# Optimization experiments

Hardware: AMD Instinct MI355X
Metric: run time of the kernel (lower is better)

The kernel has to match this reference:

```python
import jax, jax.numpy as jnp
import numpy as np

LOSS_W = 0.6
UNC_W = 0.4
EPS = 1e-8


def setup_inputs() -> dict:
    key = jax.random.key(0)
    ks = jax.random.split(key, 6)
    B, D, C, BANK = 1024, 256, 80, 65536
    return {
        "features": jax.random.normal(ks[0], (B, D), jnp.float32),
        "predictions": jax.random.normal(ks[1], (B, C), jnp.float32),
        "targets": jax.random.uniform(ks[2], (B, C), dtype=jnp.float32),
        "query": jax.random.normal(ks[3], (B, D), jnp.float32),
        "memory": jax.random.normal(ks[4], (BANK, D), jnp.float32),
        "importance_scores": jax.random.uniform(ks[5], (BANK,), dtype=jnp.float32),
        "index": BANK,  # bank pre-filled (steady state)
        "k": 8,
    }


def _difficulty(predictions, targets):
    # per-sample BCE-with-logits, mean over classes
    bce = -(targets * jax.nn.log_sigmoid(predictions)
            + (1.0 - targets) * jax.nn.log_sigmoid(-predictions))
    sl = bce.mean(axis=1)                                   # [B]
    mx = sl.max()
    sl = jnp.where(mx > 0, sl / (mx + EPS), sl)
    probs = jax.nn.sigmoid(predictions)
    confidence = jnp.abs(probs - 0.5).mean(axis=1)
    uncertainty = jnp.clip(1.0 - 2.0 * confidence, 0.0, 1.0)
    return LOSS_W * sl + UNC_W * uncertainty                # [B]


def _update(memory, importance_scores, index, features, difficulty):
    # 'hard' mode: store samples above the 0.7 difficulty quantile,
    # sequential priority (min-replacement) insertion via scan.
    bank_size = memory.shape[0]
    thr = jnp.quantile(difficulty, 0.7)
    store = difficulty > thr                                # [B] bool

    def step(carry, inp):
        mem, scores, idx = carry
        feat, score, st = inp
        fill = idx < bank_size
        min_idx = jnp.argmin(scores)
        min_score = scores[min_idx]
        widx = jnp.where(fill, idx, min_idx)
        do_write = st & (fill | (score > min_score))
        mem = mem.at[widx].set(jnp.where(do_write, feat, mem[widx]))
        scores = scores.at[widx].set(jnp.where(do_write, score, scores[widx]))
        idx = idx + jnp.where(st & fill, 1, 0).astype(idx.dtype)
        return (mem, scores, idx), None

    init = (memory, importance_scores, jnp.asarray(index, jnp.int32))
    (mem, scores, idx), _ = jax.lax.scan(step, init, (features, difficulty, store))
    return mem, scores, idx


def _l2norm(x):
    # torch F.normalize: x / max(||x||, eps)
    n = jnp.linalg.norm(x, axis=1, keepdims=True)
    return x / jnp.maximum(n, 1e-12)


def reference(features, predictions, targets, query, memory, importance_scores, index, k):
    difficulty = _difficulty(predictions, targets)
    mem, scores, idx = _update(memory, importance_scores, index, features, difficulty)
    # retrieve: bank is full (index starts at bank_size) -> valid_size == bank_size
    sim = _l2norm(query) @ _l2norm(mem).T                   # [B, BANK]
    w, ind = jax.lax.top_k(sim, k)                          # [B, k]
    weights = jax.nn.softmax(w, axis=1)                     # [B, k]
    gathered = mem[ind]                                     # [B, k, D]
    return jnp.einsum('bk,bkd->bd', weights, gathered)      # [B, D]
```

## Files before the change

### kernel.cpp

```cpp
#include <hip/hip_runtime.h>
#include <hip/hip_bf16.h>
#include <stdint.h>

#define BANK 65536
#define BQ 1024
#define DIM 256
#define NCLS 80
#define KTOP 8
#define CAND_CAP 1024
#define SCORE_CUT 0.007f
#define NSPLIT 128
#define SPLIT_ROWS 512
#define NT 8
#define TAU 0.2f
#define SCAP 96

typedef __attribute__((ext_vector_type(8))) short short8;
typedef __attribute__((ext_vector_type(4))) float f32x4;

__device__ __forceinline__ unsigned int mono_f32(float f) {
    unsigned int b = __float_as_uint(f);
    return (b & 0x80000000u) ? ~b : (b | 0x80000000u);
}
__device__ __forceinline__ float unmono_f32(unsigned int u) {
    unsigned int b = (u & 0x80000000u) ? (u & 0x7FFFFFFFu) : ~u;
    return __uint_as_float(b);
}
__device__ __forceinline__ unsigned short f2bf(float f) {
    unsigned int u = __float_as_uint(f);
    unsigned int r = ((u >> 16) & 1u) + 0x7FFFu;
    return (unsigned short)((u + r) >> 16);
}
__device__ __forceinline__ void stage16(const char* gsrc, char* ldst) {
    __builtin_amdgcn_global_load_lds(
        (const __attribute__((address_space(1))) unsigned int*)gsrc,
        (__attribute__((address_space(3))) unsigned int*)ldst, 16, 0, 0);
}

#define INS8(L, key) do { \
    _Pragma("unroll") \
    for (int pp = 7; pp >= 1; --pp) { \
        unsigned long long prev = L[pp - 1]; \
        L[pp] = (L[pp] >= (key)) ? L[pp] : ((prev >= (key)) ? (key) : prev); \
    } \
    L[0] = (L[0] >= (key)) ? L[0] : (key); \
} while (0)

__global__ void prep_all(const float* __restrict__ memory, const float* __restrict__ features,
                         const float* __restrict__ query,
                         const float* __restrict__ pred, const float* __restrict__ targ,
                         const float* __restrict__ scores,
                         unsigned short* __restrict__ Mn, unsigned short* __restrict__ Qn,
                         float* __restrict__ invm, float* __restrict__ invq,
                         float* __restrict__ sl_raw, float* __restrict__ unc,
                         int* __restrict__ ovw, unsigned long long* __restrict__ cand,
                         int* __restrict__ meta) {
    int bx = blockIdx.x;
    if (bx < 16640) {
        int wid = threadIdx.x >> 6, lane = threadIdx.x & 63;
        int row = bx * 4 + wid;
        bool isq = (row >= BANK);
        const float* src = isq ? (query + (size_t)(row - BANK) * DIM)
                               : (memory + (size_t)row * DIM);
        float4 v = *(const float4*)(src + lane * 4);
        float ss = v.x * v.x + v.y * v.y + v.z * v.z + v.w * v.w;
        for (int off = 32; off; off >>= 1) ss += __shfl_xor(ss, off);
        float inv = 1.f / fmaxf(sqrtf(ss), 1e-12f);
        ushort4 o;
        o.x = f2bf(v.x * inv); o.y = f2bf(v.y * inv);
        o.z = f2bf(v.z * inv); o.w = f2bf(v.w * inv);
        if (!isq) {
            *(ushort4*)(Mn + (size_t)row * DIM + lane * 4) = o;
            if (lane == 0) invm[row] = inv;
        } else {
            *(ushort4*)(Qn + (size_t)(row - BANK) * DIM + lane * 4) = o;
            if (lane == 0) invq[row - BANK] = inv;
        }
    } else if (bx < 16896) {
        int wid = threadIdx.x >> 6, lane = threadIdx.x & 63;
        int b = (bx - 16640) * 4 + wid;
        float bce = 0.f, conf = 0.f;
        for (int c = lane; c < NCLS; c += 64) {
            float x = pred[b * NCLS + c];
            float t = targ[b * NCLS + c];
            float l1 = log1pf(expf(-fabsf(x)));
            float sp_pos = fmaxf(x, 0.f) + l1;
            float sp_neg = fmaxf(-x, 0.f) + l1;
            bce += t * sp_neg + (1.f - t) * sp_pos;
            float p = 1.f / (1.f + expf(-x));
            conf += fabsf(p - 0.5f);
        }
        for (int off = 32; off; off >>= 1) {
            bce += __shfl_xor(bce, off);
            conf += __shfl_xor(conf, off);
        }
        if (lane == 0) {
            sl_raw[b] = bce / (float)NCLS;
            float u = 1.f - 2.f * (conf / (float)NCLS);
            unc[b] = fminf(fmaxf(u, 0.f), 1.f);
        }
    } else {
        int i = (bx - 16896) * 256 + threadIdx.x;
        ovw[i] = -1;
        float s = scores[i];
        if (s < SCORE_CUT) {
            int pos = atomicAdd(&meta[1], 1);
            if (pos < CAND_CAP)
                cand[pos] = ((unsigned long long)__float_as_uint(s) << 32) | (unsigned long long)(unsigned)i;
        }
    }
}

__global__ void select_scatter(const float* __restrict__ sl_raw, const float* __restrict__ unc,
                               const unsigned long long* __restrict__ cand,
                               int* __restrict__ meta, int* __restrict__ ovw,
                               int* __restrict__ wlist) {
    __shared__ float red[BQ];
    __shared__ int hist[1024];
    __shared__ int pfx[1024];
    __shared__ int p[BQ];
    __shared__ int sidx[BQ];
    __shared__ int fill[1024];
    __shared__ unsigned long long kc[CAND_CAP];
    __shared__ unsigned long long buck[CAND_CAP];
    __shared__ float binvals[128];
    __shared__ int bincnt;
    __shared__ int b716s, b717s;
    __shared__ float q716s, q717s;
    int tid = threadIdx.x;

    float sl = sl_raw[tid];
    float u = unc[tid];
    red[tid] = sl;
    hist[tid] = 0;
    __syncthreads();
    for (int off = 512; off; off >>= 1) {
        if (tid < off) red[tid] = fmaxf(red[tid], red[tid + off]);
        __syncthreads();
    }
    float mx = red[0];
    float sln = (mx > 0.f) ? sl / (mx + 1e-8f) : sl;
    float diff = 0.6f * sln + 0.4f * u;
    int mybin = (int)(diff * 1024.f);
    mybin = (mybin < 0) ? 0 : ((mybin > 1023) ? 1023 : mybin);
    atomicAdd(&hist[mybin], 1);
    __syncthreads();
    pfx[tid] = hist[tid];
    __syncthreads();
    for (int off = 1; off < 1024; off <<= 1) {
        int t = (tid >= off) ? pfx[tid - off] : 0;
        __syncthreads();
        pfx[tid] += t;
        __syncthreads();
    }
    int pe = pfx[tid] - hist[tid];
    if (pe <= 716 && 716 < pfx[tid]) b716s = tid;
    if (pe <= 717 && 717 < pfx[tid]) b717s = tid;
    __syncthreads();
#pragma unroll
    for (int pass = 0; pass < 2; ++pass) {
        int target = 716 + pass;
        if (tid == 0) bincnt = 0;
        __syncthreads();
        int tb = (pass == 0) ? b716s : b717s;
        if (mybin == tb) {
            int pos = atomicAdd(&bincnt, 1);
            if (pos < 128) binvals[pos] = diff;
        }
        __syncthreads();
        if (tid == 0) {
            int bc = bincnt; if (bc > 128) bc = 128;
            for (int i = 1; i < bc; ++i) {
                float v = binvals[i]; int j = i - 1;
                while (j >= 0 && binvals[j] > v) { binvals[j + 1] = binvals[j]; --j; }
                binvals[j + 1] = v;
            }
            int base = pfx[tb] - hist[tb];
            float val = binvals[target - base];
            if (pass == 0) q716s = val; else q717s = val;
        }
        __syncthreads();
    }
    float qpos = 0.7f * (float)(BQ - 1);
    float g = qpos - floorf(qpos);
    float thr = q716s + g * (q717s - q716s);
    int flag = (diff > thr) ? 1 : 0;
    p[tid] = flag;
    __syncthreads();
    for (int off = 1; off < BQ; off <<= 1) {
        int t = (tid >= off) ? p[tid - off] : 0;
        __syncthreads();
        p[tid] += t;
        __syncthreads();
    }
    if (flag) sidx[p[tid] - 1] = tid;
    __syncthreads();
    int m = p[BQ - 1];

    int n = meta[1];
    if (n > CAND_CAP) n = CAND_CAP;
    if (m > n) m = n;
    if (tid == 0) meta[2] = m;
    kc[tid] = (tid < n) ? cand[tid] : 0xFFFFFFFFFFFFFFFFull;
    hist[tid] = 0;
    fill[tid] = 0;
    __syncthreads();
    int mybin2 = 0;
    if (tid < n) {
        float s = __uint_as_float((unsigned)(kc[tid] >> 32));
        mybin2 = (int)(s * (1024.f / SCORE_CUT));
        mybin2 = (mybin2 < 0) ? 0 : ((mybin2 > 1023) ? 1023 : mybin2);
        atomicAdd(&hist[mybin2], 1);
    }
    __syncthreads();
    pfx[tid] = hist[tid];
    __syncthreads();
    for (int off = 1; off < 1024; off <<= 1) {
        int t = (tid >= off) ? pfx[tid - off] : 0;
        __syncthreads();
        pfx[tid] += t;
        __syncthreads();
    }
    if (tid < n) {
        int pe2 = pfx[mybin2] - hist[mybin2];
        int slot = pe2 + atomicAdd(&fill[mybin2], 1);
        buck[slot] = kc[tid];
    }
    __syncthreads();
    if (tid < n) {
        int pe2 = pfx[mybin2] - hist[mybin2];
        int cnt2 = hist[mybin2];
        unsigned long long me = kc[tid];
        int rank = pe2;
        for (int i = 0; i < cnt2; ++i) rank += (buck[pe2 + i] < me) ? 1 : 0;
        if (rank < m) {
            int row = (int)(unsigned)(me & 0xFFFFFFFFu);
            ovw[row] = sidx[rank];
            wlist[rank] = row;
        }
    }
}

__global__ void patch_kernel(const float* __restrict__ features, const int* __restrict__ ovw,
                             const int* __restrict__ wlist, const int* __restrict__ meta,
                             unsigned short* __restrict__ Mn, float* __restrict__ invm) {
    int wid = threadIdx.x >> 6, lane = threadIdx.x & 63;
    int j = blockIdx.x * 4 + wid;
    if (j >= meta[2]) return;
    int row = wlist[j];
    int s = ovw[row];
    const float* src = features + (size_t)s * DIM;
    float4 v = *(const float4*)(src + lane * 4);
    float ss = v.x * v.x + v.y * v.y + v.z * v.z + v.w * v.w;
    for (int off = 32; off; off >>= 1) ss += __shfl_xor(ss, off);
    float inv = 1.f / fmaxf(sqrtf(ss), 1e-12f);
    ushort4 o;
    o.x = f2bf(v.x * inv); o.y = f2bf(v.y * inv);
    o.z = f2bf(v.z * inv); o.w = f2bf(v.w * inv);
    *(ushort4*)(Mn + (size_t)row * DIM + lane * 4) = o;
    if (lane == 0) invm[row] = inv;
}

__global__ __launch_bounds__(256, 2) void sim_coarse(
    const unsigned short* __restrict__ Qn, const unsigned short* __restrict__ Mn,
    int* __restrict__ surv, int* __restrict__ cnt) {
    __shared__ char smem[2 * 32768];

    int bx = blockIdx.x;
    int qt = bx >> 7;
    int split = bx & 127;
    int tid = threadIdx.x;
    int w = tid >> 6;
    int lane = tid & 63;
    int le = lane & 15;
    int lg = lane >> 4;
    int qbase = qt * 256 + w * 64;
    int r0 = split * SPLIT_ROWS;

    short8 qf[4][8];
#pragma unroll
    for (int qg = 0; qg < 4; ++qg)
#pragma unroll
        for (int ks = 0; ks < 8; ++ks)
            qf[qg][ks] = *(const short8*)((const char*)Qn +
                (size_t)(qbase + qg * 16 + le) * 512 + ks * 64 + lg * 16);

#define STAGE_TILE(tidx, bufbase) do { \
    int _rrow0 = r0 + (tidx) * 64; \
    _Pragma("unroll") \
    for (int _i = 0; _i < 8; ++_i) { \
        int _p = _i * 4096 + tid * 16; \
        int _row = _p >> 9; \
        int _colp = _p & 511; \
        const char* _g = (const char*)Mn + (size_t)(_rrow0 + _row) * 512 + (_colp ^ ((_row & 7) << 4)); \
        stage16(_g, smem + (bufbase) + _p); \
    } \
} while (0)

    STAGE_TILE(0, 0);

    for (int t = 0; t < NT; ++t) {
        int cur = (t & 1) * 32768;
        __syncthreads();
        if (t + 1 < NT) STAGE_TILE(t + 1, 32768 - cur);

        f32x4 acc[4][4];
#pragma unroll
        for (int rg = 0; rg < 4; ++rg)
#pragma unroll
            for (int qg = 0; qg < 4; ++qg)
                acc[rg][qg] = (f32x4){0.f, 0.f, 0.f, 0.f};

#pragma unroll
        for (int ks = 0; ks < 8; ++ks) {
            int colb = (ks * 64 + lg * 16) ^ ((le & 7) << 4);
#pragma unroll
            for (int rg = 0; rg < 4; ++rg) {
                short8 af = *(const short8*)(smem + cur + (rg * 16 + le) * 512 + colb);
#pragma unroll
                for (int qg = 0; qg < 4; ++qg)
                    acc[rg][qg] = __builtin_amdgcn_mfma_f32_16x16x32_bf16(af, qf[qg][ks], acc[rg][qg], 0, 0, 0);
            }
        }

        int rbase = r0 + t * 64 + lg * 4;
#pragma unroll
        for (int rg = 0; rg < 4; ++rg) {
            int rb = rbase + rg * 16;
#pragma unroll
            for (int qg = 0; qg < 4; ++qg) {
                f32x4 a = acc[rg][qg];
                float gmax = fmaxf(fmaxf(a[0], a[1]), fmaxf(a[2], a[3]));
                if (gmax >= TAU) {
                    int q = qbase + qg * 16 + le;
#pragma unroll
                    for (int j = 0; j < 4; ++j) {
                        if (a[j] >= TAU) {
                            int pos = atomicAdd(&cnt[q], 1);
                            if (pos < SCAP) surv[q * SCAP + pos] = rb + j;
                        }
                    }
                }
            }
        }
    }
}

__global__ void rerank(const int* __restrict__ surv, const int* __restrict__ cnt,
                       const float* __restrict__ query, const float* __restrict__ features,
                       const float* __restrict__ memory, const int* __restrict__ ovw,
                       const float* __restrict__ invq, const float* __restrict__ invm,
                       float* __restrict__ out) {
    __shared__ int crow[SCAP];
    __shared__ float cval[SCAP];
    __shared__ float w8[KTOP];
    __shared__ int r8[KTOP];
    int q = blockIdx.x;
    int tid = threadIdx.x;
    int n = cnt[q]; if (n > SCAP) n = SCAP;
    for (int i = tid; i < SCAP; i += 256) crow[i] = (i < n) ? surv[q * SCAP + i] : 0;
    __syncthreads();
    int wv = tid >> 6, lane = tid & 63;
    float4 qv = *(const float4*)(query + (size_t)q * DIM + lane * 4);
    float iq = invq[q];
    for (int j0 = 0; j0 < n; j0 += 32) {
        for (int jj = 0; jj < 8; ++jj) {
            int j = j0 + wv * 8 + jj;
            if (j < n) {
                int r = crow[j];
                int s = ovw[r];
                const float* src = (s >= 0) ? (features + (size_t)s * DIM) : (memory + (size_t)r * DIM);
                float4 mv = *(const float4*)(src + lane * 4);
                float d = qv.x * mv.x + qv.y * mv.y + qv.z * mv.z + qv.w * mv.w;
                for (int off = 32; off; off >>= 1) d += __shfl_xor(d, off);
                if (lane == 0) cval[j] = d * iq * invm[r];
            }
        }
    }
    __syncthreads();
    if (tid == 0) {
        unsigned long long t8[8];
#pragma unroll
        for (int j = 0; j < 8; ++j) t8[j] = 0ull;
        for (int j = 0; j < n; ++j) {
            unsigned long long key =
                ((unsigned long long)mono_f32(cval[j]) << 32) |
                (unsigned long long)(0xFFFFFFFFu - (unsigned)crow[j]);
            if (key > t8[7]) INS8(t8, key);
        }
        float s[KTOP], e[KTOP];
        float sum = 0.f;
#pragma unroll
        for (int j = 0; j < KTOP; ++j) {
            s[j] = unmono_f32((unsigned)(t8[j] >> 32));
            int r = (int)(0xFFFFFFFFu - (unsigned)(t8[j] & 0xFFFFFFFFu));
            r8[j] = (r < 0) ? 0 : ((r >= BANK) ? 0 : r);
        }
        float mx = s[0];
#pragma unroll
        for (int j = 0; j < KTOP; ++j) { e[j] = expf(s[j] - mx); sum += e[j]; }
#pragma unroll
        for (int j = 0; j < KTOP; ++j) w8[j] = e[j] / sum;
    }
    __syncthreads();
    int d = tid;
    float accv = 0.f;
#pragma unroll
    for (int j = 0; j < KTOP; ++j) {
        int r = r8[j];
        int s2 = ovw[r];
        const float* src = (s2 >= 0) ? (features + (size_t)s2 * DIM) : (memory + (size_t)r * DIM);
        accv = fmaf(w8[j], src[d], accv);
    }
    out[(size_t)q * DIM + d] = accv;
}

extern "C" void kernel_launch(void* const* d_in, const int* in_sizes, int n_in,
                              void* d_out, int out_size, void* d_ws, size_t ws_size,
                              hipStream_t stream) {
    const float* features = (const float*)d_in[0];
    const float* predictions = (const float*)d_in[1];
    const float* targets = (const float*)d_in[2];
    const float* query = (const float*)d_in[3];
    const float* memory = (const float*)d_in[4];
    const float* scores = (const float*)d_in[5];
    float* out = (float*)d_out;

    char* ws = (char*)d_ws;
    int* cnt = (int*)(ws);
    int* meta = (int*)(ws + 4096);
    float* sl_raw = (float*)(ws + 8192);
    float* unc = (float*)(ws + 12288);
    int* wlist = (int*)(ws + 16384);
    float* invq = (float*)(ws + 20480);
    unsigned long long* cand = (unsigned long long*)(ws + 24576);
    int* surv = (int*)(ws + 32768);
    int* ovw = (int*)(ws + 425984);
    float* invm = (float*)(ws + 688128);
    unsigned short* Qn = (unsigned short*)(ws + 1048576);
    unsigned short* Mn = (unsigned short*)(ws + 2097152);

    hipMemsetAsync(ws, 0, 8192, stream);
    prep_all<<<17152, 256, 0, stream>>>(memory, features, query, predictions, targets, scores,
                                        Mn, Qn, invm, invq, sl_raw, unc, ovw, cand, meta);
    select_scatter<<<1, BQ, 0, stream>>>(sl_raw, unc, cand, meta, ovw, wlist);
    patch_kernel<<<256, 256, 0, stream>>>(features, ovw, wlist, meta, Mn, invm);
    sim_coarse<<<4 * NSPLIT, 256, 0, stream>>>(Qn, Mn, surv, cnt);
    rerank<<<BQ, 256, 0, stream>>>(surv, cnt, query, features, memory, ovw, invq, invm, out);
}
```

Baseline: 133.4 us.

## Triple-buffer smaller memory tiles with explicit vmcnt waits in coarse similarity kernel

The sim_coarse kernel moves from a double buffer of 64-row tiles to a triple buffer of 32-row tiles, with 16 tiles per split instead of 8. Prefetch now runs two tiles ahead. The single __syncthreads is replaced by an explicit s_waitcnt vmcnt(4) plus s_barrier, so loads for later tiles can stay in flight while the current tile is computed. The LDS swizzle changes from XOR to a rotation to avoid bank conflicts. This shrinks shared memory use and deepens load/compute overlap, but depends on the exact count of outstanding loads per tile and makes each tile smaller with more barriers.

```diff
diff --git a/kernel.cpp b/kernel.cpp
--- a/kernel.cpp
+++ b/kernel.cpp
@@ -11,7 +11,7 @@
 #define SCORE_CUT 0.007f
 #define NSPLIT 128
 #define SPLIT_ROWS 512
-#define NT 8
+#define NT 16
 #define TAU 0.2f
 #define SCAP 96
 
@@ -264,18 +264,19 @@
 __global__ __launch_bounds__(256, 2) void sim_coarse(
     const unsigned short* __restrict__ Qn, const unsigned short* __restrict__ Mn,
     int* __restrict__ surv, int* __restrict__ cnt) {
-    __shared__ char smem[2 * 32768];
+    __shared__ char smem[3 * 16384];
 
     int bx = blockIdx.x;
     int qt = bx >> 7;
     int split = bx & 127;
     int tid = threadIdx.x;
+    int lane = tid & 63;
     int w = tid >> 6;
-    int lane = tid & 63;
     int le = lane & 15;
     int lg = lane >> 4;
     int qbase = qt * 256 + w * 64;
     int r0 = split * SPLIT_ROWS;
+    int rot = (lg + 4 * (le & 7)) & 31;
 
     short8 qf[4][8];
 #pragma unroll
@@ -286,46 +287,58 @@
                 (size_t)(qbase + qg * 16 + le) * 512 + ks * 64 + lg * 16);
 
 #define STAGE_TILE(tidx, bufbase) do { \
-    int _rrow0 = r0 + (tidx) * 64; \
+    int _rr0 = r0 + (tidx) * 32; \
     _Pragma("unroll") \
-    for (int _i = 0; _i < 8; ++_i) { \
+    for (int _i = 0; _i < 4; ++_i) { \
         int _p = _i * 4096 + tid * 16; \
         int _row = _p >> 9; \
-        int _colp = _p & 511; \
-        const char* _g = (const char*)Mn + (size_t)(_rrow0 + _row) * 512 + (_colp ^ ((_row & 7) << 4)); \
+        int _pc = (_p >> 4) & 31; \
+        int _lc = (_pc - 4 * (_row & 7)) & 31; \
+        const char* _g = (const char*)Mn + (size_t)(_rr0 + _row) * 512 + _lc * 16; \
         stage16(_g, smem + (bufbase) + _p); \
     } \
 } while (0)
 
     STAGE_TILE(0, 0);
-
+    STAGE_TILE(1, 16384);
+
+    int cb = 0;
     for (int t = 0; t < NT; ++t) {
-        int cur = (t & 1) * 32768;
-        __syncthreads();
-        if (t + 1 < NT) STAGE_TILE(t + 1, 32768 - cur);
-
-        f32x4 acc[4][4];
-#pragma unroll
-        for (int rg = 0; rg < 4; ++rg)
+        if (t < NT - 1) {
+            asm volatile("s_waitcnt vmcnt(4)" ::: "memory");
+        } else {
+            asm volatile("s_waitcnt vmcnt(0)" ::: "memory");
+        }
+        __builtin_amdgcn_s_barrier();
+        __builtin_amdgcn_sched_barrier(0);
+        if (t + 2 < NT) {
+            int sb = cb + 2; if (sb >= 3) sb -= 3;
+            STAGE_TILE(t + 2, sb * 16384);
+        }
+        const char* base = smem + cb * 16384;
+
+        f32x4 acc[2][4];
+#pragma unroll
+        for (int rg = 0; rg < 2; ++rg)
 #pragma unroll
             for (int qg = 0; qg < 4; ++qg)
                 acc[rg][qg] = (f32x4){0.f, 0.f, 0.f, 0.f};
 
 #pragma unroll
         for (int ks = 0; ks < 8; ++ks) {
-            int colb = (ks * 64 + lg * 16) ^ ((le & 7) << 4);
-#pragma unroll
-            for (int rg = 0; rg < 4; ++rg) {
-                short8 af = *(const short8*)(smem + cur + (rg * 16 + le) * 512 + colb);
+            int colb = ((ks * 4 + rot) & 31) << 4;
+#pragma unroll
+            for (int rg = 0; rg < 2; ++rg) {
+                short8 af = *(const short8*)(base + (rg * 16 + le) * 512 + colb);
 #pragma unroll
                 for (int qg = 0; qg < 4; ++qg)
                     acc[rg][qg] = __builtin_amdgcn_mfma_f32_16x16x32_bf16(af, qf[qg][ks], acc[rg][qg], 0, 0, 0);
             }
         }
 
-        int rbase = r0 + t * 64 + lg * 4;
-#pragma unroll
-        for (int rg = 0; rg < 4; ++rg) {
+        int rbase = r0 + t * 32 + lg * 4;
+#pragma unroll
+        for (int rg = 0; rg < 2; ++rg) {
             int rb = rbase + rg * 16;
 #pragma unroll
             for (int qg = 0; qg < 4; ++qg) {
@@ -343,6 +356,7 @@
                 }
             }
         }
+        cb = (cb == 2) ? 0 : cb + 1;
     }
 }
 
```

Measured after the change: 131.5 us. No clear change (-1.4%).
